# Kernel optimization log

Hardware: AMD Instinct MI355X
Metric: run time of the kernel (lower is better)

The kernel has to match this reference:

```python
import jax, jax.numpy as jnp
import numpy as np

B, T, N, D, H = 2, 12, 1024, 128, 8
HD = D // H  # head_dim = 16


def setup_inputs() -> dict:
    key = jax.random.key(0)
    ks = jax.random.split(key, 11)
    std = 0.02
    return {
        "query": jax.random.normal(ks[0], (B, T, N, D), dtype=jnp.float32),
        "key": jax.random.normal(ks[1], (B, T, N, D), dtype=jnp.float32),
        "value": jax.random.normal(ks[2], (B, T, N, D), dtype=jnp.float32),
        "Wq": jax.random.normal(ks[3], (D, D), dtype=jnp.float32) * std,
        "bq": jnp.zeros((D,), dtype=jnp.float32),
        "Wk": jax.random.normal(ks[4], (D, D), dtype=jnp.float32) * std,
        "bk": jnp.zeros((D,), dtype=jnp.float32),
        "Wv": jax.random.normal(ks[5], (D, D), dtype=jnp.float32) * std,
        "bv": jnp.zeros((D,), dtype=jnp.float32),
        "Wo": jax.random.normal(ks[6], (D, D), dtype=jnp.float32) * std,
        "bo": jnp.zeros((D,), dtype=jnp.float32),
    }


def reference(query, key, value, Wq, bq, Wk, bk, Wv, bv, Wo, bo):
    # Linear projections (torch nn.Linear: x @ W.T + b)
    q = query @ Wq.T + bq   # (B,T,N,D)
    k = key @ Wk.T + bk
    v = value @ Wv.T + bv
    # split heads: last dim D -> (H, HD)
    q = q.reshape(B, T, N, H, HD)
    k = k.reshape(B, T, N, H, HD)
    v = v.reshape(B, T, N, H, HD)
    scale = 1.0 / jnp.sqrt(jnp.float32(HD))
    # attention across node dim (N); scores (B,H,T,N,N) ~ 805 MB
    scores = jnp.einsum('btnhd,btmhd->bhtnm', q, k) * scale
    attn = jax.nn.softmax(scores, axis=-1)
    out = jnp.einsum('bhtnm,btmhd->btnhd', attn, v)  # (B,T,N,H,HD)
    out = out.reshape(B, T, N, D)
    return out @ Wo.T + bo
```

## Files before the change

### kernel.cpp

```cpp
#include <hip/hip_runtime.h>


#define DEV __device__ __forceinline__

typedef __attribute__((ext_vector_type(4))) float f32x4;
typedef __attribute__((ext_vector_type(8))) short s16x8;
typedef __attribute__((ext_vector_type(4))) short s16x4;
typedef __attribute__((ext_vector_type(2))) unsigned int u32x2;

DEV unsigned short f2bf(float f) {
    unsigned u = __builtin_bit_cast(unsigned, f);
    u = (u + 0x7fffu + ((u >> 16) & 1u)) >> 16;
    return (unsigned short)u;
}

DEV unsigned pack_bf16(float a, float b) {
#if __has_builtin(__builtin_amdgcn_cvt_pk_bf16_f32)
    typedef __attribute__((ext_vector_type(2))) __bf16 bf16x2;
    bf16x2 t = __builtin_amdgcn_cvt_pk_bf16_f32(a, b);
    return __builtin_bit_cast(unsigned, t);
#else
    unsigned ua = __builtin_bit_cast(unsigned, a) + 0x8000u;
    unsigned ub = __builtin_bit_cast(unsigned, b) + 0x8000u;
    return __builtin_amdgcn_perm(ub, ua, 0x07060302);
#endif
}

DEV f32x4 mfma16(s16x4 a, s16x4 b, f32x4 c) {
#if __has_builtin(__builtin_amdgcn_mfma_f32_16x16x16bf16_1k)
    return __builtin_amdgcn_mfma_f32_16x16x16bf16_1k(a, b, c, 0, 0, 0);
#else
    s16x8 a8 = {a[0], a[1], a[2], a[3], 0, 0, 0, 0};
    s16x8 b8 = {b[0], b[1], b[2], b[3], 0, 0, 0, 0};
    return __builtin_amdgcn_mfma_f32_16x16x32_bf16(a8, b8, c, 0, 0, 0);
#endif
}

__global__ __launch_bounds__(256)
void qkv_proj_kernel(const float* __restrict__ xq, const float* __restrict__ xk,
                     const float* __restrict__ xv,
                     const float* __restrict__ Wq, const float* __restrict__ Wk,
                     const float* __restrict__ Wv,
                     const float* __restrict__ bq, const float* __restrict__ bk,
                     const float* __restrict__ bv,
                     unsigned short* __restrict__ oq, unsigned short* __restrict__ ok,
                     unsigned short* __restrict__ ov)
{
    const int z = blockIdx.y;
    const float* X    = (z == 0) ? xq : (z == 1) ? xk : xv;
    const float* W    = (z == 0) ? Wq : (z == 1) ? Wk : Wv;
    const float* bias = (z == 0) ? bq : (z == 1) ? bk : bv;
    unsigned short* out = (z == 0) ? oq : (z == 1) ? ok : ov;
    const float scale = (z == 0) ? 0.25f * 1.44269504088896f : 1.0f;

    __shared__ unsigned short Xs[64 * 136];
    __shared__ unsigned short Ws[128 * 136];

    const int t  = threadIdx.x;
    const int m0 = blockIdx.x * 64;

    {
        const float4* Xg = (const float4*)(X + (size_t)m0 * 128);
        #pragma unroll
        for (int p = 0; p < 8; p++) {
            int g = p * 256 + t;
            float4 vv = Xg[g];
            int row = g >> 5, c4 = g & 31;
            ushort4 d;
            d.x = f2bf(vv.x); d.y = f2bf(vv.y); d.z = f2bf(vv.z); d.w = f2bf(vv.w);
            *(ushort4*)&Xs[row * 136 + c4 * 4] = d;
        }
        const float4* Wg = (const float4*)W;
        #pragma unroll
        for (int p = 0; p < 16; p++) {
            int g = p * 256 + t;
            float4 vv = Wg[g];
            int row = g >> 5, c4 = g & 31;
            ushort4 d;
            d.x = f2bf(vv.x); d.y = f2bf(vv.y); d.z = f2bf(vv.z); d.w = f2bf(vv.w);
            *(ushort4*)&Ws[row * 136 + c4 * 4] = d;
        }
    }
    __syncthreads();

    const int wave = t >> 6, lane = t & 63, quad = lane >> 4, n16 = lane & 15;
    f32x4 acc[8];
    const f32x4 zero4 = {0.f, 0.f, 0.f, 0.f};
    #pragma unroll
    for (int i = 0; i < 8; i++) acc[i] = zero4;

    #pragma unroll
    for (int ks = 0; ks < 4; ks++) {
        s16x8 a = *(const s16x8*)&Xs[(wave * 16 + n16) * 136 + ks * 32 + quad * 8];
        #pragma unroll
        for (int nt = 0; nt < 8; nt++) {
            s16x8 b = *(const s16x8*)&Ws[(nt * 16 + n16) * 136 + ks * 32 + quad * 8];
            acc[nt] = __builtin_amdgcn_mfma_f32_16x16x32_bf16(a, b, acc[nt], 0, 0, 0);
        }
    }

    const int bt    = m0 >> 10;
    const int nbase = (m0 & 1023) + wave * 16 + quad * 4;
    if (z == 2) {
        #pragma unroll
        for (int nt = 0; nt < 8; nt++) {
            float bb = bias[nt * 16 + n16];
            u32x2 pv = {pack_bf16(acc[nt][0] + bb, acc[nt][1] + bb),
                        pack_bf16(acc[nt][2] + bb, acc[nt][3] + bb)};
            *(u32x2*)&out[((size_t)(bt * 8 + nt) * 16 + n16) * 1024 + nbase] = pv;
        }
    } else {
        #pragma unroll
        for (int nt = 0; nt < 8; nt++) {
            float bb = bias[nt * 16 + n16];
            #pragma unroll
            for (int r = 0; r < 4; r++) {
                float v = (acc[nt][r] + bb) * scale;
                out[((size_t)(bt * 8 + nt) * 1024 + (nbase + r)) * 16 + n16] = f2bf(v);
            }
        }
    }
}

__global__ __launch_bounds__(256)
void attn_kernel(const unsigned short* __restrict__ q,
                 const unsigned short* __restrict__ k,
                 const unsigned short* __restrict__ vt,
                 unsigned short* __restrict__ O)
{
    __shared__ unsigned short Ks[256 * 20];
    __shared__ unsigned short VTs[16 * 264];

    const int t    = threadIdx.x;
    const int wave = t >> 6, lane = t & 63, quad = lane >> 4, n16 = lane & 15;
    const int bx = blockIdx.x, h = blockIdx.y, bt = blockIdx.z;
    const size_t headoff = (size_t)(bt * 8 + h) * 16384;
    const int q0 = bx * 64 + wave * 16;

    s16x4 qf = *(const s16x4*)(q + headoff + (size_t)(q0 + n16) * 16 + quad * 4);

    const f32x4 zero4 = {0.f, 0.f, 0.f, 0.f};
    f32x4 oacc = zero4;
    float dp = 0.f;
    const int krd = n16 * 20 + quad * 4;
    const int vrd = n16 * 264 + quad * 4;

    for (int c = 0; c < 4; c++) {
        __syncthreads();
        #pragma unroll
        for (int p = 0; p < 4; p++) {
            int g = p * 256 + t, row = g >> 2, qq = g & 3;
            *(s16x4*)&Ks[row * 20 + qq * 4] =
                *(const s16x4*)(k + headoff + (size_t)(c * 256 + row) * 16 + qq * 4);
        }
        #pragma unroll
        for (int p = 0; p < 2; p++) {
            int g = p * 256 + t, row = g >> 5, seg = g & 31;
            *(s16x8*)&VTs[row * 264 + seg * 8] =
                *(const s16x8*)(vt + headoff + (size_t)row * 1024 + c * 256 + seg * 8);
        }
        __syncthreads();

        #pragma unroll
        for (int st = 0; st < 16; st++) {
            const int jb = st * 16;
            s16x4 kf = *(const s16x4*)&Ks[jb * 20 + krd];
            f32x4 s = mfma16(kf, qf, zero4);
            float p0 = __builtin_amdgcn_exp2f(s[0]);
            float p1 = __builtin_amdgcn_exp2f(s[1]);
            float p2 = __builtin_amdgcn_exp2f(s[2]);
            float p3 = __builtin_amdgcn_exp2f(s[3]);
            dp += (p0 + p1) + (p2 + p3);
            u32x2 pp = {pack_bf16(p0, p1), pack_bf16(p2, p3)};
            s16x4 pf = __builtin_bit_cast(s16x4, pp);
            s16x4 vf = *(const s16x4*)&VTs[jb + vrd];
            oacc = mfma16(pf, vf, oacc);
        }
    }

    dp += __shfl_xor(dp, 16);
    dp += __shfl_xor(dp, 32);

    const int orow = q0 + quad * 4;
    #pragma unroll
    for (int r = 0; r < 4; r++) {
        float d = __shfl(dp, quad * 4 + r);
        float rv = oacc[r] * __builtin_amdgcn_rcpf(d);
        O[((size_t)bt * 1024 + orow + r) * 128 + h * 16 + n16] = f2bf(rv);
    }
}

__global__ __launch_bounds__(256)
void o_proj_kernel(const unsigned short* __restrict__ X, const float* __restrict__ W,
                   const float* __restrict__ bias, float* __restrict__ out)
{
    __shared__ unsigned short Xs[64 * 136];
    __shared__ unsigned short Ws[128 * 136];

    const int t  = threadIdx.x;
    const int m0 = blockIdx.x * 64;

    {
        #pragma unroll
        for (int p = 0; p < 4; p++) {
            int g = p * 256 + t, row = g >> 4, ch = g & 15;
            *(s16x8*)&Xs[row * 136 + ch * 8] =
                *(const s16x8*)(X + (size_t)(m0 + row) * 128 + ch * 8);
        }
        const float4* Wg = (const float4*)W;
        #pragma unroll
        for (int p = 0; p < 16; p++) {
            int g = p * 256 + t;
            float4 vv = Wg[g];
            int row = g >> 5, c4 = g & 31;
            ushort4 d;
            d.x = f2bf(vv.x); d.y = f2bf(vv.y); d.z = f2bf(vv.z); d.w = f2bf(vv.w);
            *(ushort4*)&Ws[row * 136 + c4 * 4] = d;
        }
    }
    __syncthreads();

    const int wave = t >> 6, lane = t & 63, quad = lane >> 4, n16 = lane & 15;
    f32x4 acc[8];
    const f32x4 zero4 = {0.f, 0.f, 0.f, 0.f};
    #pragma unroll
    for (int i = 0; i < 8; i++) acc[i] = zero4;

    #pragma unroll
    for (int ks = 0; ks < 4; ks++) {
        s16x8 a = *(const s16x8*)&Xs[(wave * 16 + n16) * 136 + ks * 32 + quad * 8];
        #pragma unroll
        for (int nt = 0; nt < 8; nt++) {
            s16x8 b = *(const s16x8*)&Ws[(nt * 16 + n16) * 136 + ks * 32 + quad * 8];
            acc[nt] = __builtin_amdgcn_mfma_f32_16x16x32_bf16(a, b, acc[nt], 0, 0, 0);
        }
    }

    const int mrow = m0 + wave * 16 + quad * 4;
    #pragma unroll
    for (int nt = 0; nt < 8; nt++) {
        float bb = bias[nt * 16 + n16];
        #pragma unroll
        for (int r = 0; r < 4; r++)
            out[(size_t)(mrow + r) * 128 + nt * 16 + n16] = acc[nt][r] + bb;
    }
}

extern "C" void kernel_launch(void* const* d_in, const int* in_sizes, int n_in,
                              void* d_out, int out_size, void* d_ws, size_t ws_size,
                              hipStream_t stream)
{
    const float* query = (const float*)d_in[0];
    const float* key_  = (const float*)d_in[1];
    const float* value = (const float*)d_in[2];
    const float* Wq = (const float*)d_in[3];
    const float* bq = (const float*)d_in[4];
    const float* Wk = (const float*)d_in[5];
    const float* bk = (const float*)d_in[6];
    const float* Wv = (const float*)d_in[7];
    const float* bv = (const float*)d_in[8];
    const float* Wo = (const float*)d_in[9];
    const float* bo = (const float*)d_in[10];
    float* out = (float*)d_out;

    char* ws = (char*)d_ws;
    unsigned short* qb = (unsigned short*)(ws);
    unsigned short* kb = (unsigned short*)(ws + 6291456);
    unsigned short* vb = (unsigned short*)(ws + 12582912);
    unsigned short* Ob = (unsigned short*)(ws + 18874368);

    qkv_proj_kernel<<<dim3(384, 3, 1), 256, 0, stream>>>(
        query, key_, value, Wq, Wk, Wv, bq, bk, bv, qb, kb, vb);
    attn_kernel<<<dim3(16, 8, 24), 256, 0, stream>>>(qb, kb, vb, Ob);
    o_proj_kernel<<<dim3(384, 1, 1), 256, 0, stream>>>(Ob, Wo, bo, out);
}
```

Before: 153.9 us.

## Use 16x16x32 MFMA for PV with permuted K rows and MFMA row-sums

The attention inner loop now processes 32 keys per step. It permutes the K rows in shared memory so that two 16x16x16 score MFMAs produce the register layout needed by a single 16x16x32 PV MFMA. The softmax denominator is computed by an extra MFMA against a ones vector, replacing the scalar adds and cross-lane shuffles. The Q/K projection epilogue is staged through shared memory so global stores become 16-byte vectors instead of scattered 2-byte ones. The trade-off is an extra MFMA per step, two extra barriers, and the denominator now being summed from bf16-rounded probabilities.

```diff
diff --git a/kernel.cpp b/kernel.cpp
--- a/kernel.cpp
+++ b/kernel.cpp
@@ -7,6 +7,7 @@
 typedef __attribute__((ext_vector_type(8))) short s16x8;
 typedef __attribute__((ext_vector_type(4))) short s16x4;
 typedef __attribute__((ext_vector_type(2))) unsigned int u32x2;
+typedef __attribute__((ext_vector_type(4))) unsigned int u32x4;
 
 DEV unsigned short f2bf(float f) {
     unsigned u = __builtin_bit_cast(unsigned, f);
@@ -36,6 +37,10 @@
 #endif
 }
 
+DEV f32x4 mfma32(s16x8 a, s16x8 b, f32x4 c) {
+    return __builtin_amdgcn_mfma_f32_16x16x32_bf16(a, b, c, 0, 0, 0);
+}
+
 __global__ __launch_bounds__(256)
 void qkv_proj_kernel(const float* __restrict__ xq, const float* __restrict__ xk,
                      const float* __restrict__ xv,
@@ -110,14 +115,22 @@
             *(u32x2*)&out[((size_t)(bt * 8 + nt) * 16 + n16) * 1024 + nbase] = pv;
         }
     } else {
+        __syncthreads();
+        const int crow = wave * 16 + quad * 4;
         #pragma unroll
         for (int nt = 0; nt < 8; nt++) {
             float bb = bias[nt * 16 + n16];
             #pragma unroll
-            for (int r = 0; r < 4; r++) {
-                float v = (acc[nt][r] + bb) * scale;
-                out[((size_t)(bt * 8 + nt) * 1024 + (nbase + r)) * 16 + n16] = f2bf(v);
-            }
+            for (int r = 0; r < 4; r++)
+                Xs[(crow + r) * 136 + nt * 16 + n16] = f2bf((acc[nt][r] + bb) * scale);
+        }
+        __syncthreads();
+        #pragma unroll
+        for (int p = 0; p < 4; p++) {
+            int g = p * 256 + t, row = g >> 4, ch = g & 15;
+            s16x8 val = *(const s16x8*)&Xs[row * 136 + ch * 8];
+            *(s16x8*)&out[((size_t)(bt * 8 + (ch >> 1)) * 1024 + (m0 & 1023) + row) * 16
+                          + (ch & 1) * 8] = val;
         }
     }
 }
@@ -140,18 +153,21 @@
     s16x4 qf = *(const s16x4*)(q + headoff + (size_t)(q0 + n16) * 16 + quad * 4);
 
     const f32x4 zero4 = {0.f, 0.f, 0.f, 0.f};
-    f32x4 oacc = zero4;
-    float dp = 0.f;
+    f32x4 oacc = zero4, dacc = zero4;
+    const s16x8 ones = {0x3F80, 0x3F80, 0x3F80, 0x3F80,
+                        0x3F80, 0x3F80, 0x3F80, 0x3F80};
     const int krd = n16 * 20 + quad * 4;
-    const int vrd = n16 * 264 + quad * 4;
+    const int vrd = n16 * 264 + quad * 8;
 
     for (int c = 0; c < 4; c++) {
         __syncthreads();
         #pragma unroll
         for (int p = 0; p < 4; p++) {
-            int g = p * 256 + t, row = g >> 2, qq = g & 3;
-            *(s16x4*)&Ks[row * 20 + qq * 4] =
-                *(const s16x4*)(k + headoff + (size_t)(c * 256 + row) * 16 + qq * 4);
+            int g = p * 256 + t, rr = g >> 2, qq = g & 3;
+            int r5 = rr & 31;
+            int lrow = (rr & ~31) + ((r5 & 4) << 2) + ((r5 >> 3) << 2) + (r5 & 3);
+            *(s16x4*)&Ks[lrow * 20 + qq * 4] =
+                *(const s16x4*)(k + headoff + (size_t)(c * 256 + rr) * 16 + qq * 4);
         }
         #pragma unroll
         for (int p = 0; p < 2; p++) {
@@ -162,30 +178,33 @@
         __syncthreads();
 
         #pragma unroll
-        for (int st = 0; st < 16; st++) {
-            const int jb = st * 16;
-            s16x4 kf = *(const s16x4*)&Ks[jb * 20 + krd];
-            f32x4 s = mfma16(kf, qf, zero4);
-            float p0 = __builtin_amdgcn_exp2f(s[0]);
-            float p1 = __builtin_amdgcn_exp2f(s[1]);
-            float p2 = __builtin_amdgcn_exp2f(s[2]);
-            float p3 = __builtin_amdgcn_exp2f(s[3]);
-            dp += (p0 + p1) + (p2 + p3);
-            u32x2 pp = {pack_bf16(p0, p1), pack_bf16(p2, p3)};
-            s16x4 pf = __builtin_bit_cast(s16x4, pp);
-            s16x4 vf = *(const s16x4*)&VTs[jb + vrd];
-            oacc = mfma16(pf, vf, oacc);
-        }
-    }
-
-    dp += __shfl_xor(dp, 16);
-    dp += __shfl_xor(dp, 32);
+        for (int w = 0; w < 8; w++) {
+            const int jb = w * 32;
+            s16x4 kf0 = *(const s16x4*)&Ks[jb * 20 + krd];
+            s16x4 kf1 = *(const s16x4*)&Ks[(jb + 16) * 20 + krd];
+            f32x4 s0 = mfma16(kf0, qf, zero4);
+            f32x4 s1 = mfma16(kf1, qf, zero4);
+            float p0 = __builtin_amdgcn_exp2f(s0[0]);
+            float p1 = __builtin_amdgcn_exp2f(s0[1]);
+            float p2 = __builtin_amdgcn_exp2f(s0[2]);
+            float p3 = __builtin_amdgcn_exp2f(s0[3]);
+            float p4 = __builtin_amdgcn_exp2f(s1[0]);
+            float p5 = __builtin_amdgcn_exp2f(s1[1]);
+            float p6 = __builtin_amdgcn_exp2f(s1[2]);
+            float p7 = __builtin_amdgcn_exp2f(s1[3]);
+            u32x4 pp = {pack_bf16(p0, p1), pack_bf16(p2, p3),
+                        pack_bf16(p4, p5), pack_bf16(p6, p7)};
+            s16x8 pf = __builtin_bit_cast(s16x8, pp);
+            s16x8 vf = *(const s16x8*)&VTs[jb + vrd];
+            oacc = mfma32(pf, vf, oacc);
+            dacc = mfma32(pf, ones, dacc);
+        }
+    }
 
     const int orow = q0 + quad * 4;
     #pragma unroll
     for (int r = 0; r < 4; r++) {
-        float d = __shfl(dp, quad * 4 + r);
-        float rv = oacc[r] * __builtin_amdgcn_rcpf(d);
+        float rv = oacc[r] * __builtin_amdgcn_rcpf(dacc[r]);
         O[((size_t)bt * 1024 + orow + r) * 128 + h * 16 + n16] = f2bf(rv);
     }
 }
```

Result: no change. 152.4 us (-1.0%).
